# Kernel optimization log

Hardware: AMD Instinct MI355X
Metric: run time of the kernel (lower is better)

The kernel has to match this reference:

```python
import jax, jax.numpy as jnp
import numpy as np
from jax import lax

B, C, H, W = 2, 64, 192, 192
KS = 3
N = KS * KS
L = 3  # num_gdns (ResBlocks)


def conv2d(x, w, b=None, padding=0):
    out = lax.conv_general_dilated(x, w, (1, 1), [(padding, padding)] * 2,
                                   dimension_numbers=('NCHW', 'OIHW', 'NCHW'))
    if b is not None:
        out = out + b[None, :, None, None]
    return out


def gdn(x, beta, gamma):
    # y = x / sqrt(beta + sum_j gamma_ij x_j^2)  (inverse=False)
    norm = conv2d(x * x, gamma[:, :, None, None], beta)
    return x / jnp.sqrt(norm)


def resblock(x, w1, w2, beta, gamma):
    res = x
    h = jax.nn.celu(gdn(conv2d(x, w1, padding=0), beta, gamma))  # conv1: no pad (H-2)
    return conv2d(h, w2, padding=2) + res  # conv2: pad 2 restores H


def deform_conv(x, offset, w_dc):
    # DCNv1 (pure-pytorch impl): offset (b,2N,h,w), rows first then cols.
    b, c, Hh, Ww = x.shape
    h, w = offset.shape[2], offset.shape[3]
    pad = 1
    xp = jnp.pad(x, ((0, 0), (0, 0), (pad, pad), (pad, pad)))
    Hp, Wp = Hh + 2 * pad, Ww + 2 * pad
    r = (KS - 1) // 2
    knr, knc = jnp.meshgrid(jnp.arange(-r, r + 1), jnp.arange(-r, r + 1), indexing='ij')
    p_n = jnp.concatenate([knr.reshape(-1), knc.reshape(-1)]).astype(x.dtype)  # (2N,)
    gr, gc = jnp.meshgrid(jnp.arange(1, h + 1), jnp.arange(1, w + 1), indexing='ij')
    p0 = jnp.concatenate([jnp.broadcast_to(gr[None], (N, h, w)),
                          jnp.broadcast_to(gc[None], (N, h, w))], 0).astype(x.dtype)  # (2N,h,w)
    p = p0[None] + p_n[None, :, None, None] + offset  # (b,2N,h,w)
    p = jnp.transpose(p, (0, 2, 3, 1))  # (b,h,w,2N)
    pr = jnp.clip(p[..., :N], 0, Hp - 1)
    pc = jnp.clip(p[..., N:], 0, Wp - 1)
    q0 = lax.stop_gradient(jnp.floor(p))
    qr0 = jnp.clip(q0[..., :N], 0, Hp - 1).astype(jnp.int32)
    qc0 = jnp.clip(q0[..., N:], 0, Wp - 1).astype(jnp.int32)
    qr1 = jnp.clip(q0[..., :N] + 1, 0, Hp - 1).astype(jnp.int32)
    qc1 = jnp.clip(q0[..., N:] + 1, 0, Wp - 1).astype(jnp.int32)
    # bilinear weights (match torch impl exactly)
    g_lt = (1 + (qr0 - pr)) * (1 + (qc0 - pc))
    g_rb = (1 - (qr1 - pr)) * (1 - (qc1 - pc))
    g_lb = (1 + (qr0 - pr)) * (1 - (qc1 - pc))
    g_rt = (1 - (qr1 - pr)) * (1 + (qc0 - pc))
    xf = xp.reshape(b, c, Hp * Wp)

    def gather(qr, qc):
        idx = (qr * Wp + qc).reshape(b, -1)  # (b, h*w*N)
        g = jax.vmap(lambda xb, ib: xb[:, ib])(xf, idx)  # (b,c,h*w*N)
        return g.reshape(b, c, h, w, N)

    xo = (g_lt[:, None] * gather(qr0, qc0) + g_rb[:, None] * gather(qr1, qc1)
          + g_lb[:, None] * gather(qr0, qc1) + g_rt[:, None] * gather(qr1, qc0))
    # stride-ks conv over reshaped x_offset == contraction over (c, n)
    wf = w_dc.reshape(w_dc.shape[0], c, N)
    return jnp.einsum('bchwn,ocn->bohw', xo, wf)


def setup_inputs() -> dict:
    key = jax.random.key(0)
    ks = jax.random.split(key, 11)
    f_r = jax.random.normal(ks[0], (B, C, H, W), jnp.float32)
    m_t = jax.random.normal(ks[1], (B, C, H, W), jnp.float32)
    w_pconv = jax.random.normal(ks[2], (2 * N, C, KS, KS), jnp.float32) * 0.01
    b_pconv = jax.random.normal(ks[3], (2 * N,), jnp.float32) * 0.01
    w_dc = jax.random.normal(ks[4], (C, C, KS, KS), jnp.float32) * 0.05
    w_cat = jax.random.normal(ks[5], (C, 2 * C, KS, KS), jnp.float32) * 0.05
    b_cat = jax.random.normal(ks[6], (C,), jnp.float32) * 0.05
    rb_w1 = jax.random.normal(ks[7], (L, C, C, KS, KS), jnp.float32) * 0.01
    rb_w2 = jax.random.normal(ks[8], (L, C, C, KS, KS), jnp.float32) * 0.01
    rb_beta = jax.random.uniform(ks[9], (L, C), jnp.float32) * 0.5 + 0.5
    rb_gamma = jnp.broadcast_to(0.1 * jnp.eye(C, dtype=jnp.float32), (L, C, C)) \
        + jax.random.uniform(ks[10], (L, C, C), jnp.float32) * 0.01
    return {"f_r": f_r, "m_t": m_t, "w_pconv": w_pconv, "b_pconv": b_pconv,
            "w_dc": w_dc, "w_cat": w_cat, "b_cat": b_cat,
            "rb_w1": rb_w1, "rb_w2": rb_w2, "rb_beta": rb_beta, "rb_gamma": rb_gamma}


def reference(f_r, m_t, w_pconv, b_pconv, w_dc, w_cat, b_cat, rb_w1, rb_w2, rb_beta, rb_gamma):
    offset = conv2d(m_t, w_pconv, b_pconv, padding=1)  # (B, 2N, H, W)
    x = deform_conv(f_r, offset, w_dc)                  # (B, C, H, W)
    y = conv2d(jnp.concatenate([x, f_r], axis=1), w_cat, b_cat, padding=1)
    for i in range(L):
        y = resblock(y, rb_w1[i], rb_w2[i], rb_beta[i], rb_gamma[i])
    return y + x
```

## Files before the change

### kernel.cpp

```cpp
#include <hip/hip_runtime.h>

typedef __attribute__((ext_vector_type(8))) __bf16 bf16x8;
typedef __attribute__((ext_vector_type(4))) __bf16 bf16x4;
typedef __attribute__((ext_vector_type(16))) float f32x16;
typedef __attribute__((ext_vector_type(4))) float f32x4;
typedef __attribute__((ext_vector_type(4))) int i32x4;

#define HH 192
#define WW 192
#define HW 36864
#define HW1 36100

#define TCS 144
#define RP66 (66 * TCS)
#define GDNPITCH 144
#define TREG 8704

__device__ inline f32x16 mfma32(bf16x8 a, bf16x8 b, f32x16 c) {
  return __builtin_amdgcn_mfma_f32_32x32x16_bf16(a, b, c, 0, 0, 0);
}

__device__ inline f32x16 zero16() {
  f32x16 z;
#pragma unroll
  for (int e = 0; e < 16; ++e) z[e] = 0.f;
  return z;
}

__global__ __launch_bounds__(256) void prep_weights(
    const float* __restrict__ wp, const float* __restrict__ bp,
    const float* __restrict__ wdc, const float* __restrict__ wcat,
    const float* __restrict__ w1, const float* __restrict__ w2,
    const float* __restrict__ gamma,
    __bf16* __restrict__ wpA, __bf16* __restrict__ wdcA,
    __bf16* __restrict__ wcatA, __bf16* __restrict__ w1A,
    __bf16* __restrict__ w2A, __bf16* __restrict__ gA,
    float* __restrict__ bpad) {
  int i = blockIdx.x * 256 + threadIdx.x;
  if (i < 18432) {
    int j = i & 7, lane = (i >> 3) & 63, kc = (i >> 9) & 3, n = i >> 11;
    int o = lane & 31, c = kc * 16 + ((lane >> 5) << 3) + j;
    wpA[i] = (o < 18) ? (__bf16)wp[(o * 64 + c) * 9 + n] : (__bf16)0.f;
    return;
  }
  i -= 18432;
  if (i < 36864) {
    int j = i & 7, lane = (i >> 3) & 63, ot = (i >> 9) & 1, kc = (i >> 10) & 3, n = i >> 12;
    int o = ot * 32 + (lane & 31), c = kc * 16 + ((lane >> 5) << 3) + j;
    wdcA[i] = (__bf16)wdc[(o * 64 + c) * 9 + n];
    return;
  }
  i -= 36864;
  if (i < 73728) {
    int d = i, j = d & 7; d >>= 3; int lane = d & 63; d >>= 6; int ot = d & 1; d >>= 1;
    int kc = d & 7; int n = d >> 3;
    int o = ot * 32 + (lane & 31), c = kc * 16 + ((lane >> 5) << 3) + j;
    wcatA[i] = (__bf16)wcat[(o * 128 + c) * 9 + n];
    return;
  }
  i -= 73728;
  if (i < 110592) {
    int l = i / 36864, di = i % 36864, d = di;
    int j = d & 7; d >>= 3; int lane = d & 63; d >>= 6; int ot = d & 1; d >>= 1;
    int kc = d & 3; int n = d >> 2;
    int o = ot * 32 + (lane & 31), c = kc * 16 + ((lane >> 5) << 3) + j;
    w1A[l * 36864 + di] = (__bf16)w1[l * 36864 + (o * 64 + c) * 9 + n];
    return;
  }
  i -= 110592;
  if (i < 110592) {
    int l = i / 36864, di = i % 36864, d = di;
    int j = d & 7; d >>= 3; int lane = d & 63; d >>= 6; int ot = d & 1; d >>= 1;
    int kc = d & 3; int n = d >> 2;
    int o = ot * 32 + (lane & 31), c = kc * 16 + ((lane >> 5) << 3) + j;
    w2A[l * 36864 + di] = (__bf16)w2[l * 36864 + (o * 64 + c) * 9 + n];
    return;
  }
  i -= 110592;
  if (i < 12288) {
    int l = i / 4096, di = i % 4096, d = di;
    int j = d & 7; d >>= 3; int lane = d & 63; d >>= 6; int ot = d & 1; d >>= 1;
    int kc = d & 3;
    int o = ot * 32 + (lane & 31), c = kc * 16 + ((lane >> 5) << 3) + j;
    gA[l * 4096 + di] = (__bf16)gamma[l * 4096 + o * 64 + c];
    return;
  }
  i -= 12288;
  if (i < 20) bpad[i] = (i < 18) ? bp[i] : 0.f;
}

__global__ __launch_bounds__(256) void to_nhwc_bf16(
    const float* __restrict__ fr, const float* __restrict__ mt,
    __bf16* __restrict__ frn, __bf16* __restrict__ mtn) {
  __shared__ __align__(16) __bf16 tile[64 * 72];
  int tensor = blockIdx.x / 1152, rem = blockIdx.x % 1152;
  int b = rem / 576, p0 = (rem % 576) * 64;
  const float* src = (tensor ? mt : fr) + (size_t)b * 64 * HW;
  __bf16* dst = (tensor ? mtn : frn) + (size_t)b * HW * 64;
  int tid = threadIdx.x, c = tid >> 2, q0 = (tid & 3) * 16;
  const float* sp = src + (size_t)c * HW + p0 + q0;
#pragma unroll
  for (int qq = 0; qq < 4; ++qq) {
    f32x4 v = *(const f32x4*)(sp + qq * 4);
#pragma unroll
    for (int e = 0; e < 4; ++e) tile[(q0 + qq * 4 + e) * 72 + c] = (__bf16)v[e];
  }
  __syncthreads();
  int px = tid >> 2, c0 = (tid & 3) * 16;
  bf16x8 a = *(const bf16x8*)(&tile[px * 72 + c0]);
  bf16x8 b8 = *(const bf16x8*)(&tile[px * 72 + c0 + 8]);
  __bf16* dp = dst + (size_t)(p0 + px) * 64 + c0;
  *(bf16x8*)dp = a;
  *(bf16x8*)(dp + 8) = b8;
}

template <int ROWS, int COLS, int TPB>
__device__ inline void stage_bf16T(const __bf16* __restrict__ src,
                                   int srcH, int srcW, int row0, int col0,
                                   unsigned char* lds) {
  for (int i = threadIdx.x; i < ROWS * COLS * 8; i += TPB) {
    int r = i / (COLS * 8), rem = i - r * (COLS * 8), j = rem >> 3, u = rem & 7;
    int gr = row0 + r, gc = col0 + j;
    bf16x8 v;
#pragma unroll
    for (int e = 0; e < 8; ++e) v[e] = (__bf16)0.f;
    if (gr >= 0 && gr < srcH && gc >= 0 && gc < srcW)
      v = *(const bf16x8*)(src + ((size_t)gr * srcW + gc) * 64 + u * 8);
    *(bf16x8*)(lds + r * (COLS * TCS) + j * TCS + u * 16) = v;
  }
}

template <int KC, int KOFFA, bool EDGE>
__device__ inline void kloopG(const __bf16* __restrict__ wA,
                              const __bf16* __restrict__ src,
                              int H, int W, int P, int h0, int w0,
                              f32x16 acc[2][2]) {
  const int lane = threadIdx.x & 63;
  const int m = lane & 31, half = lane >> 5;
  const __bf16* aB = wA + lane * 8;
#pragma unroll
  for (int kh = 0; kh < 3; ++kh) {
#pragma unroll
    for (int kw = 0; kw < 3; ++kw) {
      const int n = kh * 3 + kw;
      int gr0 = h0 - P + kh, gr1 = gr0 + 1;
      int gc = w0 - P + kw + m;
      bool ok0 = true, ok1 = true;
      if (EDGE) {
        bool okc = (unsigned)gc < (unsigned)W;
        ok0 = okc && ((unsigned)gr0 < (unsigned)H);
        ok1 = okc && ((unsigned)gr1 < (unsigned)H);
        gc = min(max(gc, 0), W - 1);
        gr0 = min(max(gr0, 0), H - 1);
        gr1 = min(max(gr1, 0), H - 1);
      }
      const __bf16* p0 = src + ((size_t)gr0 * W + gc) * 64 + half * 8;
      const __bf16* p1 = src + ((size_t)gr1 * W + gc) * 64 + half * 8;
#pragma unroll
      for (int kc = 0; kc < 4; ++kc) {
        bf16x8 a0 = *(const bf16x8*)(aB + ((n * KC + KOFFA + kc) * 2 + 0) * 512);
        bf16x8 a1 = *(const bf16x8*)(aB + ((n * KC + KOFFA + kc) * 2 + 1) * 512);
        bf16x8 b0 = *(const bf16x8*)(p0 + kc * 16);
        bf16x8 b1 = *(const bf16x8*)(p1 + kc * 16);
        if (EDGE && !ok0) {
#pragma unroll
          for (int e = 0; e < 8; ++e) b0[e] = (__bf16)0.f;
        }
        if (EDGE && !ok1) {
#pragma unroll
          for (int e = 0; e < 8; ++e) b1[e] = (__bf16)0.f;
        }
        acc[0][0] = mfma32(a0, b0, acc[0][0]);
        acc[0][1] = mfma32(a0, b1, acc[0][1]);
        acc[1][0] = mfma32(a1, b0, acc[1][0]);
        acc[1][1] = mfma32(a1, b1, acc[1][1]);
      }
    }
  }
}

__device__ inline void acchalf_to_lds(const f32x16 acc[2][2], int pt, unsigned char* reg) {
  int lane = threadIdx.x & 63;
  int colb = lane & 31, half = lane >> 5;
#pragma unroll
  for (int ot = 0; ot < 2; ++ot)
#pragma unroll
    for (int g = 0; g < 4; ++g) {
      int o = ot * 32 + half * 4 + g * 8;
      f32x4 v;
      v[0] = acc[ot][pt][g * 4 + 0]; v[1] = acc[ot][pt][g * 4 + 1];
      v[2] = acc[ot][pt][g * 4 + 2]; v[3] = acc[ot][pt][g * 4 + 3];
      *(f32x4*)(reg + (colb * 68 + o) * 4) = v;
    }
}

__device__ inline void read_half(const unsigned char* reg, f32x4 v[8]) {
  int lane = threadIdx.x & 63;
  int col = lane & 31, ch = (lane >> 5) * 32;
#pragma unroll
  for (int q = 0; q < 8; ++q)
    v[q] = *(const f32x4*)(reg + (col * 68 + ch + q * 4) * 4);
}

__device__ inline void acc32_to_lds(const f32x16 acc[2], unsigned char* reg) {
  int lane = threadIdx.x & 63;
  int colb = lane & 31, half = lane >> 5;
#pragma unroll
  for (int ot = 0; ot < 2; ++ot)
#pragma unroll
    for (int g = 0; g < 4; ++g) {
      int o = ot * 32 + half * 4 + g * 8;
      f32x4 v;
      v[0] = acc[ot][g * 4 + 0]; v[1] = acc[ot][g * 4 + 1];
      v[2] = acc[ot][g * 4 + 2]; v[3] = acc[ot][g * 4 + 3];
      *(f32x4*)(reg + (colb * 68 + o) * 4) = v;
    }
}

__global__ __launch_bounds__(256, 1) void pconv_mfma(
    const __bf16* __restrict__ mtn, const __bf16* __restrict__ wpA,
    const float* __restrict__ bpad, float* __restrict__ off20) {
  __shared__ __align__(16) unsigned char smem[6 * RP66];
  int b = blockIdx.x / 144, r = blockIdx.x % 144, rt = r / 3, ct = r % 3;
  int h0 = rt * 4, w0 = ct * 64;
  int wid = threadIdx.x >> 6, lane = threadIdx.x & 63;
  int colb = lane & 31, half = lane >> 5, kh8 = half << 3;
  stage_bf16T<6, 66, 256>(mtn + (size_t)b * HW * 64, 192, 192, h0 - 1, w0 - 1, smem);
  const __bf16* aB = wpA + lane * 8;
  bf16x8 pcur[4], pnxt[4];
#pragma unroll
  for (int kc = 0; kc < 4; ++kc) pcur[kc] = *(const bf16x8*)(aB + kc * 512);
  __syncthreads();
  f32x16 acc[2];
  acc[0] = zero16(); acc[1] = zero16();
  {
    const unsigned char* bB = smem + wid * RP66 + colb * TCS + kh8 * 2;
#pragma unroll
    for (int n = 0; n < 9; ++n) {
      if (n < 8) {
#pragma unroll
        for (int kc = 0; kc < 4; ++kc)
          pnxt[kc] = *(const bf16x8*)(aB + ((n + 1) * 4 + kc) * 512);
      }
      const int kh = n / 3, kw = n % 3;
#pragma unroll
      for (int kc = 0; kc < 4; ++kc) {
        const unsigned char* bp = bB + kh * RP66 + kw * TCS + kc * 32;
        bf16x8 b0 = *(const bf16x8*)(bp);
        bf16x8 b1 = *(const bf16x8*)(bp + 32 * TCS);
        acc[0] = mfma32(pcur[kc], b0, acc[0]);
        acc[1] = mfma32(pcur[kc], b1, acc[1]);
      }
#pragma unroll
      for (int kc = 0; kc < 4; ++kc) pcur[kc] = pnxt[kc];
    }
  }
  __syncthreads();
  unsigned char* reg = smem + wid * 9216;
#pragma unroll
  for (int pt = 0; pt < 2; ++pt)
#pragma unroll
    for (int g = 0; g < 4; ++g) {
      int o = half * 4 + g * 8;
      f32x4 v;
      v[0] = acc[pt][g * 4 + 0]; v[1] = acc[pt][g * 4 + 1];
      v[2] = acc[pt][g * 4 + 2]; v[3] = acc[pt][g * 4 + 3];
      *(f32x4*)(reg + ((pt * 32 + colb) * 36 + o) * 4) = v;
    }
  __builtin_amdgcn_s_waitcnt(0);
  size_t pix = (size_t)b * HW + (size_t)(h0 + wid) * 192 + w0 + lane;
#pragma unroll
  for (int q = 0; q < 5; ++q) {
    f32x4 v = *(const f32x4*)(reg + (lane * 36 + q * 4) * 4);
    v += *(const f32x4*)(bpad + q * 4);
    *(f32x4*)(off20 + pix * 20 + q * 4) = v;
  }
}

#define GOPITCH 32
#define DTBL (9 * 32 * GOPITCH)
#define DBUF 4608
#define DLDS (DTBL + 2 * DBUF)
__global__ __launch_bounds__(128, 2) void deform_mfma(
    const __bf16* __restrict__ frn, const float* __restrict__ off20,
    const __bf16* __restrict__ wdcA, float* __restrict__ xlow,
    __bf16* __restrict__ xlowb) {
  __shared__ __align__(16) unsigned char smem[DLDS];
  int bid = (blockIdx.x & 7) * 288 + (blockIdx.x >> 3);
  int b = bid / 1152, r = bid % 1152;
  int h = r / 6, s = r % 6;
  int w0 = s * 32;
  int tid = threadIdx.x;
  int wid = tid >> 6, lane = tid & 63;
  int m = lane & 31, half = lane >> 5;
  int pxg = lane >> 3, slot = lane & 7;
  const __bf16* xb = frn + (size_t)b * HW * 64;
  {
    int px = tid & 31, g = tid >> 5;
    int w = w0 + px;
    size_t pixl = (size_t)b * HW + (size_t)h * 192 + w;
    const float* ofp = off20 + pixl * 20;
    for (int n = g; n < 9; n += 4) {
      float offr = ofp[n], offc = ofp[9 + n];
      float pr = (float)(h + 1 + n / 3 - 1) + offr;
      float pc = (float)(w + 1 + n % 3 - 1) + offc;
      float prc = fminf(fmaxf(pr, 0.f), 193.f);
      float pcc = fminf(fmaxf(pc, 0.f), 193.f);
      float f0r = floorf(pr), f0c = floorf(pc);
      int qr0 = (int)fminf(fmaxf(f0r, 0.f), 193.f);
      int qc0 = (int)fminf(fmaxf(f0c, 0.f), 193.f);
      int qr1 = (int)fminf(fmaxf(f0r + 1.f, 0.f), 193.f);
      int qc1 = (int)fminf(fmaxf(f0c + 1.f, 0.f), 193.f);
      float dr0 = 1.f + ((float)qr0 - prc);
      float dr1 = 1.f - ((float)qr1 - prc);
      float dc0 = 1.f + ((float)qc0 - pcc);
      float dc1 = 1.f - ((float)qc1 - pcc);
      int o0, o1, o2, o3; float g0, g1, g2, g3;
      { bool v = (qr0 >= 1 && qr0 <= 192 && qc0 >= 1 && qc0 <= 192);
        o0 = min(max(qr0-1,0),191)*WW + min(max(qc0-1,0),191); g0 = v ? dr0*dc0 : 0.f; }
      { bool v = (qr1 >= 1 && qr1 <= 192 && qc1 >= 1 && qc1 <= 192);
        o1 = min(max(qr1-1,0),191)*WW + min(max(qc1-1,0),191); g1 = v ? dr1*dc1 : 0.f; }
      { bool v = (qr0 >= 1 && qr0 <= 192 && qc1 >= 1 && qc1 <= 192);
        o2 = min(max(qr0-1,0),191)*WW + min(max(qc1-1,0),191); g2 = v ? dr0*dc1 : 0.f; }
      { bool v = (qr1 >= 1 && qr1 <= 192 && qc0 >= 1 && qc0 <= 192);
        o3 = min(max(qr1-1,0),191)*WW + min(max(qc0-1,0),191); g3 = v ? dr1*dc0 : 0.f; }
      unsigned char* dst = smem + (n * 32 + px) * GOPITCH;
      f32x4 gv; gv[0] = g0; gv[1] = g1; gv[2] = g2; gv[3] = g3;
      i32x4 ov; ov[0] = o0; ov[1] = o1; ov[2] = o2; ov[3] = o3;
      *(f32x4*)dst = gv;
      *(i32x4*)(dst + 16) = ov;
    }
  }
  __syncthreads();
  f32x16 acc[2];
  acc[0] = zero16(); acc[1] = zero16();
  const __bf16* aB = wdcA + lane * 8;
  unsigned char* buf = smem + DTBL + wid * DBUF;
  const unsigned char* bB = buf + m * TCS + (half << 3) * 2;
  int n0 = wid ? 0 : 5, nn = wid ? 5 : 4;

  bf16x8 C[4][4];
  f32x4 G[4];
  bf16x8 a[8];

  auto load_tap = [&](int n) {
#pragma unroll
    for (int i = 0; i < 4; ++i) {
      const unsigned char* gp = smem + (size_t)(n * 32 + i * 8 + pxg) * GOPITCH;
      i32x4 oi = *(const i32x4*)(gp + 16);
      G[i] = *(const f32x4*)gp;
#pragma unroll
      for (int j = 0; j < 4; ++j)
        C[i][j] = *(const bf16x8*)(xb + (size_t)oi[j] * 64 + slot * 8);
    }
  };
  auto load_a = [&](int n) {
#pragma unroll
    for (int kc = 0; kc < 4; ++kc) {
      a[kc * 2 + 0] = *(const bf16x8*)(aB + ((n * 4 + kc) * 2 + 0) * 512);
      a[kc * 2 + 1] = *(const bf16x8*)(aB + ((n * 4 + kc) * 2 + 1) * 512);
    }
  };
  auto blend_write = [&]() {
#pragma unroll
    for (int i = 0; i < 4; ++i) {
      bf16x8 ov;
#pragma unroll
      for (int e = 0; e < 8; ++e) {
        float f = G[i][0] * (float)C[i][0][e] + G[i][1] * (float)C[i][1][e] +
                  G[i][2] * (float)C[i][2][e] + G[i][3] * (float)C[i][3][e];
        ov[e] = (__bf16)f;
      }
      *(bf16x8*)(buf + (i * 8 + pxg) * TCS + slot * 16) = ov;
    }
  };
  auto consume = [&]() {
#pragma unroll
    for (int kc = 0; kc < 4; ++kc) {
      bf16x8 b0 = *(const bf16x8*)(bB + kc * 32);
      acc[0] = mfma32(a[kc * 2 + 0], b0, acc[0]);
      acc[1] = mfma32(a[kc * 2 + 1], b0, acc[1]);
    }
  };

  load_tap(n0);
  blend_write();
  for (int t = 1; t < nn; ++t) {
    load_a(n0 + t - 1);
    load_tap(n0 + t);
    consume();
    asm volatile("s_waitcnt lgkmcnt(0)" ::: "memory");
    blend_write();
  }
  load_a(n0 + nn - 1);
  consume();
  __syncthreads();
  unsigned char* reg = smem;
  if (wid == 1) acc32_to_lds(acc, reg);
  __syncthreads();
  if (wid == 0) {
    int colb = m;
#pragma unroll
    for (int ot = 0; ot < 2; ++ot)
#pragma unroll
      for (int g = 0; g < 4; ++g) {
        int o = ot * 32 + half * 4 + g * 8;
        f32x4 v = *(const f32x4*)(reg + (colb * 68 + o) * 4);
        v[0] += acc[ot][g * 4 + 0]; v[1] += acc[ot][g * 4 + 1];
        v[2] += acc[ot][g * 4 + 2]; v[3] += acc[ot][g * 4 + 3];
        *(f32x4*)(reg + (colb * 68 + o) * 4) = v;
      }
    __builtin_amdgcn_s_waitcnt(0);
    int ch = half * 32;
    size_t pix = (size_t)b * HW + (size_t)h * 192 + w0 + colb;
    float* dp = xlow + pix * 64 + ch;
    __bf16* dpb = xlowb + pix * 64 + ch;
#pragma unroll
    for (int q = 0; q < 8; ++q) {
      f32x4 v = *(const f32x4*)(reg + (colb * 68 + ch + q * 4) * 4);
      *(f32x4*)(dp + q * 4) = v;
      bf16x4 o8;
#pragma unroll
      for (int e = 0; e < 4; ++e) o8[e] = (__bf16)v[e];
      *(bf16x4*)(dpb + q * 4) = o8;
    }
  }
}

__global__ __launch_bounds__(64) void convcat_mfma(
    const __bf16* __restrict__ xlowb, const __bf16* __restrict__ frn,
    const __bf16* __restrict__ wA, const float* __restrict__ bias,
    __bf16* __restrict__ y) {
  __shared__ __align__(16) unsigned char smem[TREG];
  int bid = (blockIdx.x & 7) * 144 + (blockIdx.x >> 3);
  int b = bid / 576, r = bid % 576, rt = r / 6, ct = r % 6;
  int h0 = rt * 2, w0 = ct * 32;
  int lane = threadIdx.x & 63;
  int m = lane & 31;
  f32x16 acc[2][2];
  acc[0][0] = zero16(); acc[0][1] = zero16(); acc[1][0] = zero16(); acc[1][1] = zero16();
  const __bf16* xb = xlowb + (size_t)b * HW * 64;
  const __bf16* fb = frn + (size_t)b * HW * 64;
  bool edge = (rt == 0) || (rt == 95) || (ct == 0) || (ct == 5);
  if (edge) {
    kloopG<8, 0, true>(wA, xb, 192, 192, 1, h0, w0, acc);
    kloopG<8, 4, true>(wA, fb, 192, 192, 1, h0, w0, acc);
  } else {
    kloopG<8, 0, false>(wA, xb, 192, 192, 1, h0, w0, acc);
    kloopG<8, 4, false>(wA, fb, 192, 192, 1, h0, w0, acc);
  }
  unsigned char* reg = smem;
  int colb = m, ch = (lane >> 5) * 32;
#pragma unroll
  for (int pt = 0; pt < 2; ++pt) {
    acchalf_to_lds(acc, pt, reg);
    __builtin_amdgcn_s_waitcnt(0);
    f32x4 v[8];
    read_half(reg, v);
    int row = h0 + pt;
    __bf16* dp = y + ((size_t)b * HW + (size_t)row * 192 + w0 + colb) * 64 + ch;
#pragma unroll
    for (int q = 0; q < 8; ++q) {
      v[q] += *(const f32x4*)(bias + ch + q * 4);
      bf16x4 o;
#pragma unroll
      for (int e = 0; e < 4; ++e) o[e] = (__bf16)v[q][e];
      *(bf16x4*)(dp + q * 4) = o;
    }
    __builtin_amdgcn_s_waitcnt(0);
  }
}

__global__ __launch_bounds__(64) void conv1gdn_mfma(
    const __bf16* __restrict__ y, const __bf16* __restrict__ w1A,
    const __bf16* __restrict__ gA, const float* __restrict__ beta,
    __bf16* __restrict__ hbuf) {
  __shared__ __align__(16) unsigned char smem[9216 + TREG];
  int bid = (blockIdx.x & 7) * 144 + (blockIdx.x >> 3);
  int b = bid / 576, r = bid % 576, rt = r / 6, ct = r % 6;
  int h0 = rt * 2, w0 = ct * 32;
  int lane = threadIdx.x & 63;
  int m = lane & 31, half = lane >> 5, kh8 = half << 3;
  int colb = m;
  f32x16 acc[2][2];
  acc[0][0] = zero16(); acc[0][1] = zero16(); acc[1][0] = zero16(); acc[1][1] = zero16();
  kloopG<4, 0, false>(w1A, y + (size_t)b * HW * 64, 192, 192, 0, h0, w0, acc);
  unsigned char* gdnreg = smem;
#pragma unroll
  for (int ot = 0; ot < 2; ++ot)
#pragma unroll
    for (int pt = 0; pt < 2; ++pt)
#pragma unroll
      for (int g = 0; g < 4; ++g) {
        int o = ot * 32 + half * 4 + g * 8;
        int p = pt * 32 + colb;
        bf16x4 s;
#pragma unroll
        for (int e = 0; e < 4; ++e) {
          float x = acc[ot][pt][g * 4 + e];
          s[e] = (__bf16)(x * x);
        }
        *(bf16x4*)(gdnreg + p * GDNPITCH + o * 2) = s;
      }
  __builtin_amdgcn_s_waitcnt(0);
  f32x16 nacc[2][2];
  nacc[0][0] = zero16(); nacc[0][1] = zero16(); nacc[1][0] = zero16(); nacc[1][1] = zero16();
  {
    const __bf16* gaB = gA + lane * 8;
    const unsigned char* gb = gdnreg + colb * GDNPITCH + kh8 * 2;
#pragma unroll
    for (int kc = 0; kc < 4; ++kc) {
      bf16x8 ga0 = *(const bf16x8*)(gaB + (kc * 2 + 0) * 512);
      bf16x8 ga1 = *(const bf16x8*)(gaB + (kc * 2 + 1) * 512);
      bf16x8 b0 = *(const bf16x8*)(gb + kc * 32);
      bf16x8 b1 = *(const bf16x8*)(gb + 32 * GDNPITCH + kc * 32);
      nacc[0][0] = mfma32(ga0, b0, nacc[0][0]);
      nacc[0][1] = mfma32(ga0, b1, nacc[0][1]);
      nacc[1][0] = mfma32(ga1, b0, nacc[1][0]);
      nacc[1][1] = mfma32(ga1, b1, nacc[1][1]);
    }
  }
#pragma unroll
  for (int ot = 0; ot < 2; ++ot)
#pragma unroll
    for (int g = 0; g < 4; ++g) {
      f32x4 bet = *(const f32x4*)(beta + ot * 32 + half * 4 + g * 8);
#pragma unroll
      for (int pt = 0; pt < 2; ++pt)
#pragma unroll
        for (int e = 0; e < 4; ++e) {
          float nv = bet[e] + nacc[ot][pt][g * 4 + e];
          float hv = acc[ot][pt][g * 4 + e] * rsqrtf(nv);
          hv = hv > 0.f ? hv : expf(hv) - 1.f;
          acc[ot][pt][g * 4 + e] = hv;
        }
    }
  __builtin_amdgcn_s_waitcnt(0);
  unsigned char* reg = smem + 9216;
  int ch = half * 32;
#pragma unroll
  for (int pt = 0; pt < 2; ++pt) {
    acchalf_to_lds(acc, pt, reg);
    __builtin_amdgcn_s_waitcnt(0);
    f32x4 v[8];
    read_half(reg, v);
    int hr = h0 + pt, wcol = w0 + colb;
    if (hr < 190 && wcol < 190) {
      __bf16* dp = hbuf + ((size_t)b * HW1 + (size_t)hr * 190 + wcol) * 64 + ch;
#pragma unroll
      for (int q = 0; q < 8; ++q) {
        bf16x4 o;
#pragma unroll
        for (int e = 0; e < 4; ++e) o[e] = (__bf16)v[q][e];
        *(bf16x4*)(dp + q * 4) = o;
      }
    }
    __builtin_amdgcn_s_waitcnt(0);
  }
}

template <bool LAST>
__global__ __launch_bounds__(64) void conv2_mfma(
    const __bf16* __restrict__ hbuf, const __bf16* __restrict__ w2A,
    const float* __restrict__ xlow, __bf16* __restrict__ y,
    float* __restrict__ out) {
  __shared__ __align__(16) unsigned char smem[TREG];
  int bid = (blockIdx.x & 7) * 144 + (blockIdx.x >> 3);
  int b = bid / 576, r = bid % 576, rt = r / 6, ct = r % 6;
  int h0 = rt * 2, w0 = ct * 32;
  int lane = threadIdx.x & 63;
  int m = lane & 31;
  int colb = m, ch = (lane >> 5) * 32;
  f32x16 acc[2][2];
  acc[0][0] = zero16(); acc[0][1] = zero16(); acc[1][0] = zero16(); acc[1][1] = zero16();
  const __bf16* hb = hbuf + (size_t)b * HW1 * 64;
  bool edge = (rt == 0) || (rt == 95) || (ct == 0) || (ct == 5);
  if (edge)
    kloopG<4, 0, true>(w2A, hb, 190, 190, 2, h0, w0, acc);
  else
    kloopG<4, 0, false>(w2A, hb, 190, 190, 2, h0, w0, acc);
  unsigned char* reg = smem;
#pragma unroll
  for (int pt = 0; pt < 2; ++pt) {
    acchalf_to_lds(acc, pt, reg);
    __builtin_amdgcn_s_waitcnt(0);
    f32x4 v[8];
    read_half(reg, v);
    int row = h0 + pt;
    size_t pix = (size_t)b * HW + (size_t)row * 192 + w0 + colb;
    __bf16* yp = y + pix * 64 + ch;
#pragma unroll
    for (int q = 0; q < 8; ++q) {
      bf16x4 yv = *(const bf16x4*)(yp + q * 4);
#pragma unroll
      for (int e = 0; e < 4; ++e) v[q][e] += (float)yv[e];
    }
    if (!LAST) {
#pragma unroll
      for (int q = 0; q < 8; ++q) {
        bf16x4 o;
#pragma unroll
        for (int e = 0; e < 4; ++e) o[e] = (__bf16)v[q][e];
        *(bf16x4*)(yp + q * 4) = o;
      }
    } else {
      const float* xp = xlow + pix * 64 + ch;
#pragma unroll
      for (int q = 0; q < 8; ++q) v[q] += *(const f32x4*)(xp + q * 4);
#pragma unroll
      for (int q = 0; q < 8; ++q)
        *(f32x4*)(reg + (colb * 68 + ch + q * 4) * 4) = v[q];
      __builtin_amdgcn_s_waitcnt(0);
      int o = lane;
      float* op = out + ((size_t)b * 64 + o) * HW + (size_t)row * 192 + w0;
#pragma unroll
      for (int q = 0; q < 8; ++q) {
        f32x4 s;
#pragma unroll
        for (int e = 0; e < 4; ++e)
          s[e] = *(const float*)(reg + ((q * 4 + e) * 68 + o) * 4);
        *(f32x4*)(op + q * 4) = s;
      }
    }
    __builtin_amdgcn_s_waitcnt(0);
  }
}

extern "C" void kernel_launch(void* const* d_in, const int* in_sizes, int n_in,
                              void* d_out, int out_size, void* d_ws, size_t ws_size,
                              hipStream_t stream) {
  const float* f_r      = (const float*)d_in[0];
  const float* m_t      = (const float*)d_in[1];
  const float* w_pconv  = (const float*)d_in[2];
  const float* b_pconv  = (const float*)d_in[3];
  const float* w_dc     = (const float*)d_in[4];
  const float* w_cat    = (const float*)d_in[5];
  const float* b_cat    = (const float*)d_in[6];
  const float* rb_w1    = (const float*)d_in[7];
  const float* rb_w2    = (const float*)d_in[8];
  const float* rb_beta  = (const float*)d_in[9];
  const float* rb_gamma = (const float*)d_in[10];
  float* out = (float*)d_out;

  float* ws = (float*)d_ws;
  float*  xlow  = ws;
  __bf16* ybuf  = (__bf16*)(xlow + 4718592);
  __bf16* xlowb = (__bf16*)(xlow + 4718592 + 2359296);
  float*  off20 = xlow + 4718592 + 4718592;
  __bf16* frn   = (__bf16*)(off20 + 1474560);
  __bf16* mtn   = (__bf16*)(off20 + 1474560 + 2359296);
  __bf16* hbuf  = mtn;
  float*  wbase = off20 + 1474560 + 2359296 + 2359296;
  __bf16* wpA   = (__bf16*)wbase;
  __bf16* wdcA  = (__bf16*)(wbase + 9216);
  __bf16* wcatA = (__bf16*)(wbase + 27648);
  __bf16* w1A   = (__bf16*)(wbase + 64512);
  __bf16* w2A   = (__bf16*)(wbase + 119808);
  __bf16* gA    = (__bf16*)(wbase + 175104);
  float*  bpad  = wbase + 181248;

  prep_weights<<<1417, 256, 0, stream>>>(w_pconv, b_pconv, w_dc, w_cat, rb_w1, rb_w2,
                                         rb_gamma, wpA, wdcA, wcatA, w1A, w2A, gA, bpad);
  to_nhwc_bf16<<<2304, 256, 0, stream>>>(f_r, m_t, frn, mtn);
  pconv_mfma<<<288, 256, 0, stream>>>(mtn, wpA, bpad, off20);
  deform_mfma<<<2304, 128, 0, stream>>>(frn, off20, wdcA, xlow, xlowb);
  convcat_mfma<<<1152, 64, 0, stream>>>(xlowb, frn, wcatA, b_cat, ybuf);
  for (int l = 0; l < 3; ++l) {
    conv1gdn_mfma<<<1152, 64, 0, stream>>>(ybuf, w1A + l * 36864, gA + l * 4096,
                                           rb_beta + l * 64, hbuf);
    if (l < 2)
      conv2_mfma<false><<<1152, 64, 0, stream>>>(hbuf, w2A + l * 36864, xlow, ybuf, out);
    else
      conv2_mfma<true><<<1152, 64, 0, stream>>>(hbuf, w2A + l * 36864, xlow, ybuf, out);
  }
}
```

Before: 319.7 us.

## Double-buffer tap loads in conv kernels and redirect padding reads to zero buffer

Replaces the per-tap load-then-MFMA loop with a software-pipelined scheme that prefetches the next tap's weight and activation fragments into a second register set while the current tap's MFMAs run. Out-of-bounds taps now read from a small zeroed buffer (the bias pad area, extended to 96 entries) instead of having their values masked, which removes the separate edge/interior code paths. Launch bounds are set to one block minimum, letting the compiler use more registers for the doubled fragment buffers. This trades lower occupancy and higher register pressure for better latency hiding within each wave.

```diff
diff --git a/kernel.cpp b/kernel.cpp
--- a/kernel.cpp
+++ b/kernel.cpp
@@ -86,7 +86,7 @@
     return;
   }
   i -= 12288;
-  if (i < 20) bpad[i] = (i < 18) ? bp[i] : 0.f;
+  if (i < 96) bpad[i] = (i < 18) ? bp[i] : 0.f;
 }
 
 __global__ __launch_bounds__(256) void to_nhwc_bf16(
@@ -130,52 +130,40 @@
   }
 }
 
-template <int KC, int KOFFA, bool EDGE>
-__device__ inline void kloopG(const __bf16* __restrict__ wA,
-                              const __bf16* __restrict__ src,
-                              int H, int W, int P, int h0, int w0,
-                              f32x16 acc[2][2]) {
+template <int KC, int KOFFA, bool CLAMP>
+__device__ inline void tap_load(const __bf16* __restrict__ aB,
+                                const __bf16* __restrict__ src,
+                                const __bf16* __restrict__ zptr,
+                                int H, int W, int P, int h0, int w0, int n,
+                                bf16x8 a[8], bf16x8 b[8]) {
   const int lane = threadIdx.x & 63;
   const int m = lane & 31, half = lane >> 5;
-  const __bf16* aB = wA + lane * 8;
-#pragma unroll
-  for (int kh = 0; kh < 3; ++kh) {
-#pragma unroll
-    for (int kw = 0; kw < 3; ++kw) {
-      const int n = kh * 3 + kw;
-      int gr0 = h0 - P + kh, gr1 = gr0 + 1;
-      int gc = w0 - P + kw + m;
-      bool ok0 = true, ok1 = true;
-      if (EDGE) {
-        bool okc = (unsigned)gc < (unsigned)W;
-        ok0 = okc && ((unsigned)gr0 < (unsigned)H);
-        ok1 = okc && ((unsigned)gr1 < (unsigned)H);
-        gc = min(max(gc, 0), W - 1);
-        gr0 = min(max(gr0, 0), H - 1);
-        gr1 = min(max(gr1, 0), H - 1);
-      }
-      const __bf16* p0 = src + ((size_t)gr0 * W + gc) * 64 + half * 8;
-      const __bf16* p1 = src + ((size_t)gr1 * W + gc) * 64 + half * 8;
-#pragma unroll
-      for (int kc = 0; kc < 4; ++kc) {
-        bf16x8 a0 = *(const bf16x8*)(aB + ((n * KC + KOFFA + kc) * 2 + 0) * 512);
-        bf16x8 a1 = *(const bf16x8*)(aB + ((n * KC + KOFFA + kc) * 2 + 1) * 512);
-        bf16x8 b0 = *(const bf16x8*)(p0 + kc * 16);
-        bf16x8 b1 = *(const bf16x8*)(p1 + kc * 16);
-        if (EDGE && !ok0) {
-#pragma unroll
-          for (int e = 0; e < 8; ++e) b0[e] = (__bf16)0.f;
-        }
-        if (EDGE && !ok1) {
-#pragma unroll
-          for (int e = 0; e < 8; ++e) b1[e] = (__bf16)0.f;
-        }
-        acc[0][0] = mfma32(a0, b0, acc[0][0]);
-        acc[0][1] = mfma32(a0, b1, acc[0][1]);
-        acc[1][0] = mfma32(a1, b0, acc[1][0]);
-        acc[1][1] = mfma32(a1, b1, acc[1][1]);
-      }
-    }
+  const int kh = n / 3, kw = n % 3;
+  int gr0 = h0 - P + kh, gr1 = gr0 + 1;
+  int gc = w0 - P + kw + m;
+  const __bf16* p0 = src + ((size_t)gr0 * W + gc) * 64 + half * 8;
+  const __bf16* p1 = src + ((size_t)gr1 * W + gc) * 64 + half * 8;
+  if (CLAMP) {
+    bool okc = (unsigned)gc < (unsigned)W;
+    if (!(okc && (unsigned)gr0 < (unsigned)H)) p0 = zptr;
+    if (!(okc && (unsigned)gr1 < (unsigned)H)) p1 = zptr;
+  }
+#pragma unroll
+  for (int kc = 0; kc < 4; ++kc) {
+    a[kc * 2 + 0] = *(const bf16x8*)(aB + ((n * KC + KOFFA + kc) * 2 + 0) * 512);
+    a[kc * 2 + 1] = *(const bf16x8*)(aB + ((n * KC + KOFFA + kc) * 2 + 1) * 512);
+    b[kc * 2 + 0] = *(const bf16x8*)(p0 + kc * 16);
+    b[kc * 2 + 1] = *(const bf16x8*)(p1 + kc * 16);
+  }
+}
+
+__device__ inline void tap_mfma(const bf16x8 a[8], const bf16x8 b[8], f32x16 acc[2][2]) {
+#pragma unroll
+  for (int kc = 0; kc < 4; ++kc) {
+    acc[0][0] = mfma32(a[kc * 2 + 0], b[kc * 2 + 0], acc[0][0]);
+    acc[0][1] = mfma32(a[kc * 2 + 0], b[kc * 2 + 1], acc[0][1]);
+    acc[1][0] = mfma32(a[kc * 2 + 1], b[kc * 2 + 0], acc[1][0]);
+    acc[1][1] = mfma32(a[kc * 2 + 1], b[kc * 2 + 1], acc[1][1]);
   }
 }
 
@@ -427,27 +415,34 @@
   }
 }
 
-__global__ __launch_bounds__(64) void convcat_mfma(
+__global__ __launch_bounds__(64, 1) void convcat_mfma(
     const __bf16* __restrict__ xlowb, const __bf16* __restrict__ frn,
     const __bf16* __restrict__ wA, const float* __restrict__ bias,
-    __bf16* __restrict__ y) {
+    const __bf16* __restrict__ zptr, __bf16* __restrict__ y) {
   __shared__ __align__(16) unsigned char smem[TREG];
   int bid = (blockIdx.x & 7) * 144 + (blockIdx.x >> 3);
   int b = bid / 576, r = bid % 576, rt = r / 6, ct = r % 6;
   int h0 = rt * 2, w0 = ct * 32;
   int lane = threadIdx.x & 63;
   int m = lane & 31;
+  const __bf16* aB = wA + lane * 8;
+  const __bf16* xb = xlowb + (size_t)b * HW * 64;
+  const __bf16* fb = frn + (size_t)b * HW * 64;
   f32x16 acc[2][2];
   acc[0][0] = zero16(); acc[0][1] = zero16(); acc[1][0] = zero16(); acc[1][1] = zero16();
-  const __bf16* xb = xlowb + (size_t)b * HW * 64;
-  const __bf16* fb = frn + (size_t)b * HW * 64;
-  bool edge = (rt == 0) || (rt == 95) || (ct == 0) || (ct == 5);
-  if (edge) {
-    kloopG<8, 0, true>(wA, xb, 192, 192, 1, h0, w0, acc);
-    kloopG<8, 4, true>(wA, fb, 192, 192, 1, h0, w0, acc);
-  } else {
-    kloopG<8, 0, false>(wA, xb, 192, 192, 1, h0, w0, acc);
-    kloopG<8, 4, false>(wA, fb, 192, 192, 1, h0, w0, acc);
+  bf16x8 a[2][8], bb[2][8];
+  tap_load<8, 0, true>(aB, xb, zptr, 192, 192, 1, h0, w0, 0, a[0], bb[0]);
+#pragma unroll
+  for (int t = 0; t < 18; ++t) {
+    const int cur = t & 1, nxt = cur ^ 1;
+    if (t < 17) {
+      const int tn = t + 1;
+      if (tn < 9)
+        tap_load<8, 0, true>(aB, xb, zptr, 192, 192, 1, h0, w0, tn, a[nxt], bb[nxt]);
+      else
+        tap_load<8, 4, true>(aB, fb, zptr, 192, 192, 1, h0, w0, tn - 9, a[nxt], bb[nxt]);
+    }
+    tap_mfma(a[cur], bb[cur], acc);
   }
   unsigned char* reg = smem;
   int colb = m, ch = (lane >> 5) * 32;
@@ -471,7 +466,7 @@
   }
 }
 
-__global__ __launch_bounds__(64) void conv1gdn_mfma(
+__global__ __launch_bounds__(64, 1) void conv1gdn_mfma(
     const __bf16* __restrict__ y, const __bf16* __restrict__ w1A,
     const __bf16* __restrict__ gA, const float* __restrict__ beta,
     __bf16* __restrict__ hbuf) {
@@ -482,9 +477,19 @@
   int lane = threadIdx.x & 63;
   int m = lane & 31, half = lane >> 5, kh8 = half << 3;
   int colb = m;
+  const __bf16* aB = w1A + lane * 8;
+  const __bf16* yb = y + (size_t)b * HW * 64;
   f32x16 acc[2][2];
   acc[0][0] = zero16(); acc[0][1] = zero16(); acc[1][0] = zero16(); acc[1][1] = zero16();
-  kloopG<4, 0, false>(w1A, y + (size_t)b * HW * 64, 192, 192, 0, h0, w0, acc);
+  bf16x8 a[2][8], bb[2][8];
+  tap_load<4, 0, false>(aB, yb, nullptr, 192, 192, 0, h0, w0, 0, a[0], bb[0]);
+#pragma unroll
+  for (int t = 0; t < 9; ++t) {
+    const int cur = t & 1, nxt = cur ^ 1;
+    if (t < 8)
+      tap_load<4, 0, false>(aB, yb, nullptr, 192, 192, 0, h0, w0, t + 1, a[nxt], bb[nxt]);
+    tap_mfma(a[cur], bb[cur], acc);
+  }
   unsigned char* gdnreg = smem;
 #pragma unroll
   for (int ot = 0; ot < 2; ++ot)
@@ -560,10 +565,10 @@
 }
 
 template <bool LAST>
-__global__ __launch_bounds__(64) void conv2_mfma(
+__global__ __launch_bounds__(64, 1) void conv2_mfma(
     const __bf16* __restrict__ hbuf, const __bf16* __restrict__ w2A,
-    const float* __restrict__ xlow, __bf16* __restrict__ y,
-    float* __restrict__ out) {
+    const float* __restrict__ xlow, const __bf16* __restrict__ zptr,
+    __bf16* __restrict__ y, float* __restrict__ out) {
   __shared__ __align__(16) unsigned char smem[TREG];
   int bid = (blockIdx.x & 7) * 144 + (blockIdx.x >> 3);
   int b = bid / 576, r = bid % 576, rt = r / 6, ct = r % 6;
@@ -571,14 +576,19 @@
   int lane = threadIdx.x & 63;
   int m = lane & 31;
   int colb = m, ch = (lane >> 5) * 32;
+  const __bf16* aB = w2A + lane * 8;
+  const __bf16* hb = hbuf + (size_t)b * HW1 * 64;
   f32x16 acc[2][2];
   acc[0][0] = zero16(); acc[0][1] = zero16(); acc[1][0] = zero16(); acc[1][1] = zero16();
-  const __bf16* hb = hbuf + (size_t)b * HW1 * 64;
-  bool edge = (rt == 0) || (rt == 95) || (ct == 0) || (ct == 5);
-  if (edge)
-    kloopG<4, 0, true>(w2A, hb, 190, 190, 2, h0, w0, acc);
-  else
-    kloopG<4, 0, false>(w2A, hb, 190, 190, 2, h0, w0, acc);
+  bf16x8 a[2][8], bb[2][8];
+  tap_load<4, 0, true>(aB, hb, zptr, 190, 190, 2, h0, w0, 0, a[0], bb[0]);
+#pragma unroll
+  for (int t = 0; t < 9; ++t) {
+    const int cur = t & 1, nxt = cur ^ 1;
+    if (t < 8)
+      tap_load<4, 0, true>(aB, hb, zptr, 190, 190, 2, h0, w0, t + 1, a[nxt], bb[nxt]);
+    tap_mfma(a[cur], bb[cur], acc);
+  }
   unsigned char* reg = smem;
 #pragma unroll
   for (int pt = 0; pt < 2; ++pt) {
@@ -658,19 +668,20 @@
   __bf16* w2A   = (__bf16*)(wbase + 119808);
   __bf16* gA    = (__bf16*)(wbase + 175104);
   float*  bpad  = wbase + 181248;
+  const __bf16* zpad = (const __bf16*)(bpad + 32);
 
   prep_weights<<<1417, 256, 0, stream>>>(w_pconv, b_pconv, w_dc, w_cat, rb_w1, rb_w2,
                                          rb_gamma, wpA, wdcA, wcatA, w1A, w2A, gA, bpad);
   to_nhwc_bf16<<<2304, 256, 0, stream>>>(f_r, m_t, frn, mtn);
   pconv_mfma<<<288, 256, 0, stream>>>(mtn, wpA, bpad, off20);
   deform_mfma<<<2304, 128, 0, stream>>>(frn, off20, wdcA, xlow, xlowb);
-  convcat_mfma<<<1152, 64, 0, stream>>>(xlowb, frn, wcatA, b_cat, ybuf);
+  convcat_mfma<<<1152, 64, 0, stream>>>(xlowb, frn, wcatA, b_cat, zpad, ybuf);
   for (int l = 0; l < 3; ++l) {
     conv1gdn_mfma<<<1152, 64, 0, stream>>>(ybuf, w1A + l * 36864, gA + l * 4096,
                                            rb_beta + l * 64, hbuf);
     if (l < 2)
-      conv2_mfma<false><<<1152, 64, 0, stream>>>(hbuf, w2A + l * 36864, xlow, ybuf, out);
+      conv2_mfma<false><<<1152, 64, 0, stream>>>(hbuf, w2A + l * 36864, xlow, zpad, ybuf, out);
     else
-      conv2_mfma<true><<<1152, 64, 0, stream>>>(hbuf, w2A + l * 36864, xlow, ybuf, out);
-  }
-}
+      conv2_mfma<true><<<1152, 64, 0, stream>>>(hbuf, w2A + l * 36864, xlow, zpad, ybuf, out);
+  }
+}
```

Result: no change. 313.8 us (-1.8%).
